# Kernel tuning notes

Hardware: AMD Instinct MI355X
Metric: run time of the kernel (lower is better)

## Reference

```python
import jax, jax.numpy as jnp
import numpy as np


def setup_inputs() -> dict:
    key = jax.random.key(0)
    k1, k2 = jax.random.split(key)
    N, C, H, W = 1, 32, 128, 240
    return {
        "left_feature": jax.random.normal(k1, (N, C, H, W), dtype=jnp.float32),
        "right_feature": jax.random.normal(k2, (N, C, H, W), dtype=jnp.float32),
        "max_disparity": 192,
    }


def reference(left_feature, right_feature, max_disparity):
    # left_feature, right_feature: (N, C, H, W)
    N, C, H, W = left_feature.shape
    D4 = max_disparity // 4
    i_idx = jnp.arange(D4)[:, None]          # (D4, 1) disparity index
    w_idx = jnp.arange(W)[None, :]           # (1, W)  column index
    valid = (w_idx >= i_idx)                 # (D4, W): cols written at disparity i
    m = valid[None, None, :, None, :]        # (1, 1, D4, 1, W)

    # Left half: cost[:, :C, i, :, i:] = left[:, :, :, i:] (unshifted, masked)
    left_vol = jnp.where(m, left_feature[:, :, None, :, :], jnp.zeros((), left_feature.dtype))

    # Right half: cost[:, C:, i, :, i:] = right[:, :, :, :-i] -> right shifted by i
    shift = jnp.clip(w_idx - i_idx, 0, W - 1)              # (D4, W)
    right_sh = right_feature[:, :, :, shift]               # (N, C, H, D4, W)
    right_vol = jnp.where(m, jnp.transpose(right_sh, (0, 1, 3, 2, 4)),
                          jnp.zeros((), right_feature.dtype))

    # (N, 2C, D4, H, W)
    return jnp.concatenate([left_vol, right_vol], axis=1)
```

## Files before the change

kernel.cpp:

```cpp
#include <hip/hip_runtime.h>


constexpr int C  = 32;
constexpr int H  = 128;
constexpr int W  = 240;
constexpr int D4 = 48;
constexpr int W4 = W / 4;

typedef float f32x4 __attribute__((ext_vector_type(4)));

__device__ __forceinline__ int pidx(int w) { return w + (w >> 5); }

__global__ void __launch_bounds__(256) cost_volume_kernel(
    const float* __restrict__ left,
    const float* __restrict__ right,
    float* __restrict__ out) {
    __shared__ float row[W + (W >> 5)];

    const int blk = blockIdx.x;
    const int h   = blk & (H - 1);
    const int c2  = blk >> 7;
    const bool is_left = (c2 < C);
    const float* __restrict__ src =
        is_left ? (left  + (c2 * H + h) * W)
                : (right + ((c2 - C) * H + h) * W);

    const int tid = threadIdx.x;
    if (tid < W) row[pidx(tid)] = src[tid];
    __syncthreads();

    const int lane = tid & 63;
    const int wave = tid >> 6;
    if (lane >= W4) return;

    const int w0 = lane * 4;
    f32x4* __restrict__ out4 = reinterpret_cast<f32x4*>(out);
    const int base    = (c2 * D4 * H + h) * W4 + lane;
    const int dstride = H * W4;

#pragma unroll
    for (int pass = 0; pass < D4 / 4; ++pass) {
        const int d     = pass * 4 + wave;
        const int shift = is_left ? 0 : d;
        f32x4 v;
#pragma unroll
        for (int j = 0; j < 4; ++j) {
            const int wj = w0 + j;
            v[j] = (wj >= d) ? row[pidx(wj - shift)] : 0.0f;
        }
        __builtin_nontemporal_store(v, out4 + base + d * dstride);
    }
}

extern "C" void kernel_launch(void* const* d_in, const int* in_sizes, int n_in,
                              void* d_out, int out_size, void* d_ws,
                              size_t ws_size, hipStream_t stream) {
    const float* left  = (const float*)d_in[0];
    const float* right = (const float*)d_in[1];
    float* out = (float*)d_out;

    const int grid  = 2 * C * H;
    const int block = 256;
    cost_volume_kernel<<<grid, block, 0, stream>>>(left, right, out);
}
```

Baseline: 77.43 us.

## Map each block to a contiguous output slice and drop LDS staging

Blocks now each produce one full (channel, disparity) H×W output slice, with flat contiguous vector stores, in place of one input row fanned out across all disparities. The shared-memory row buffer and its barrier are removed, and inputs are read straight from global memory, relying on cache for the reuse across disparities. This targets store coalescing and the idle lanes left when 60 of 64 lanes were active. The cost is more global and L2 reads, plus unaligned scalar loads for the shifted right half.

```diff
diff --git a/kernel.cpp b/kernel.cpp
--- a/kernel.cpp
+++ b/kernel.cpp
@@ -1,54 +1,61 @@
 #include <hip/hip_runtime.h>
 
 
-constexpr int C  = 32;
-constexpr int H  = 128;
-constexpr int W  = 240;
-constexpr int D4 = 48;
-constexpr int W4 = W / 4;
+constexpr int C      = 32;
+constexpr int H      = 128;
+constexpr int W      = 240;
+constexpr int D4     = 48;
+constexpr int W4     = W / 4;
+constexpr int SLICE4 = H * W4;
+constexpr int BLOCK  = 256;
+constexpr int ITERS  = SLICE4 / BLOCK;
 
 typedef float f32x4 __attribute__((ext_vector_type(4)));
-
-__device__ __forceinline__ int pidx(int w) { return w + (w >> 5); }
 
 __global__ void __launch_bounds__(256) cost_volume_kernel(
     const float* __restrict__ left,
     const float* __restrict__ right,
     float* __restrict__ out) {
-    __shared__ float row[W + (W >> 5)];
+    const int slice = blockIdx.x;
+    const int d     = slice % D4;
+    const int c2    = slice / D4;
+    const bool is_left = (c2 < C);
 
-    const int blk = blockIdx.x;
-    const int h   = blk & (H - 1);
-    const int c2  = blk >> 7;
-    const bool is_left = (c2 < C);
-    const float* __restrict__ src =
-        is_left ? (left  + (c2 * H + h) * W)
-                : (right + ((c2 - C) * H + h) * W);
+    f32x4* __restrict__ out4 =
+        reinterpret_cast<f32x4*>(out) + (long)slice * SLICE4;
+    const int tid = threadIdx.x;
 
-    const int tid = threadIdx.x;
-    if (tid < W) row[pidx(tid)] = src[tid];
-    __syncthreads();
-
-    const int lane = tid & 63;
-    const int wave = tid >> 6;
-    if (lane >= W4) return;
-
-    const int w0 = lane * 4;
-    f32x4* __restrict__ out4 = reinterpret_cast<f32x4*>(out);
-    const int base    = (c2 * D4 * H + h) * W4 + lane;
-    const int dstride = H * W4;
-
+    if (is_left) {
+        const f32x4* __restrict__ src4 =
+            reinterpret_cast<const f32x4*>(left + c2 * H * W);
+#pragma unroll 6
+        for (int it = 0; it < ITERS; ++it) {
+            const int flat = it * BLOCK + tid;
+            const int w0   = (flat % W4) * 4;
+            f32x4 v = src4[flat];
+            if (w0 < d) {
 #pragma unroll
-    for (int pass = 0; pass < D4 / 4; ++pass) {
-        const int d     = pass * 4 + wave;
-        const int shift = is_left ? 0 : d;
-        f32x4 v;
+                for (int j = 0; j < 4; ++j)
+                    if (w0 + j < d) v[j] = 0.0f;
+            }
+            __builtin_nontemporal_store(v, out4 + flat);
+        }
+    } else {
+        const float* __restrict__ src = right + (c2 - C) * H * W;
+#pragma unroll 6
+        for (int it = 0; it < ITERS; ++it) {
+            const int flat = it * BLOCK + tid;
+            const int h    = flat / W4;
+            const int w0   = (flat % W4) * 4;
+            const float* __restrict__ row = src + h * W - d;
+            f32x4 v;
 #pragma unroll
-        for (int j = 0; j < 4; ++j) {
-            const int wj = w0 + j;
-            v[j] = (wj >= d) ? row[pidx(wj - shift)] : 0.0f;
+            for (int j = 0; j < 4; ++j) {
+                const int wj = w0 + j;
+                v[j] = (wj >= d) ? row[wj] : 0.0f;
+            }
+            __builtin_nontemporal_store(v, out4 + flat);
         }
-        __builtin_nontemporal_store(v, out4 + base + d * dstride);
     }
 }
 
@@ -59,7 +66,6 @@
     const float* right = (const float*)d_in[1];
     float* out = (float*)d_out;
 
-    const int grid  = 2 * C * H;
-    const int block = 256;
-    cost_volume_kernel<<<grid, block, 0, stream>>>(left, right, out);
+    const int grid = 2 * C * D4;
+    cost_volume_kernel<<<grid, BLOCK, 0, stream>>>(left, right, out);
 }
```

Measured after the change: 89.61 us. 15.7% more time.
